# Kernel tuning notes

Hardware: AMD Instinct MI355X
Metric: run time of the kernel (lower is better)

Reference implementation:

```python
import jax, jax.numpy as jnp
import numpy as np

B, N, F_IN = 8, 4096, 32
NRP = 1024
D_MODEL = 512
K = 64  # max_num_neighbors
STAGE_CFG = ((1024, 0.05), (256, 0.3), (64, 0.5))  # (num_samples=ceil(0.25*N_in), radius)


def fps(pos, m):
    """Farthest point sampling of m points from pos (N,3), deterministic start at 0."""
    d = jnp.sum((pos - pos[0]) ** 2, axis=-1)
    idxs = jnp.zeros((m,), jnp.int32)
    def body(i, carry):
        idxs, d = carry
        nxt = jnp.argmax(d).astype(jnp.int32)
        d = jnp.minimum(d, jnp.sum((pos - pos[nxt]) ** 2, axis=-1))
        return (idxs.at[i].set(nxt), d)
    idxs, _ = jax.lax.fori_loop(1, m, body, (idxs, d))
    return idxs


def apply_mlp(h, ws, bs):
    for w, b in zip(ws[:-1], bs[:-1]):
        h = jax.nn.relu(h @ w + b)
    return h @ ws[-1] + bs[-1]


def sa_stage(x, pos, m, r, ws, bs):
    """SAModule: FPS -> radius neighbors (<=K) -> PointNetConv (gather, MLP, max-scatter)."""
    idx = jax.vmap(lambda p: fps(p, m))(pos)                          # (B,m)
    pos_s = jnp.take_along_axis(pos, idx[..., None], axis=1)          # (B,m,3)
    d2 = jnp.sum((pos_s[:, :, None, :] - pos[:, None, :, :]) ** 2, -1)  # (B,m,N)
    neg = jnp.where(d2 <= r * r, -d2, -jnp.inf)
    vals, nbr = jax.lax.top_k(neg, K)                                 # (B,m,K) nearest within r
    valid = vals > -jnp.inf                                           # self always valid (d2=0)
    x_j = jax.vmap(lambda xb, nb: xb[nb])(x, nbr)                     # (B,m,K,F) gather
    p_j = jax.vmap(lambda pb, nb: pb[nb])(pos, nbr)                   # (B,m,K,3)
    h = jnp.concatenate([x_j, p_j - pos_s[:, :, None, :]], axis=-1)   # message input
    h = apply_mlp(h, ws, bs)
    h = jnp.where(valid[..., None], h, -jnp.inf)
    return jnp.max(h, axis=2), pos_s                                  # max aggregation


def _forward(point_cloud_features, point_cloud, emb_table, point_id_emb, stage_params):
    x = emb_table[point_cloud_features[..., 0]]                       # (B,N,F_IN)
    x = x.at[:, :NRP].add(point_id_emb)
    pos = point_cloud
    for (m, r), (ws, bs) in zip(STAGE_CFG, stage_params):
        x, pos = sa_stage(x, pos, m, r, ws, bs)
    return x, pos                                                     # (B,64,D_MODEL), (B,64,3)


def setup_inputs() -> dict:
    key = jax.random.key(0)
    ks = iter(jax.random.split(key, 64))
    def nrm(shape, s=0.05):
        return s * jax.random.normal(next(ks), shape, dtype=jnp.float32)
    inp = {
        "point_cloud_features": jax.random.randint(next(ks), (B, N, 1), 0, 3),
        "point_cloud": jax.random.uniform(next(ks), (B, N, 3), dtype=jnp.float32),
        "emb_table": nrm((3, F_IN), 1.0),
        "point_id_emb": nrm((1, NRP, F_IN), 1.0),
    }
    dims = {"s1": [3 + F_IN, 64, 64, 64], "s2": [64 + 3, 128, 128, 256], "s3": [256 + 3, 256, 512, D_MODEL]}
    for s, d in dims.items():
        for i in range(3):
            inp[f"{s}w{i}"] = nrm((d[i], d[i + 1]))
            inp[f"{s}b{i}"] = jnp.zeros((d[i + 1],), jnp.float32)
    return inp


def reference(point_cloud_features, point_cloud, emb_table, point_id_emb,
              s1w0, s1b0, s1w1, s1b1, s1w2, s1b2,
              s2w0, s2b0, s2w1, s2b1, s2w2, s2b2,
              s3w0, s3b0, s3w1, s3b1, s3w2, s3b2):
    stage_params = [
        ([s1w0, s1w1, s1w2], [s1b0, s1b1, s1b2]),
        ([s2w0, s2w1, s2w2], [s2b0, s2b1, s2b2]),
        ([s3w0, s3w1, s3w2], [s3b0, s3b1, s3b2]),
    ]
    return _forward(point_cloud_features, point_cloud, emb_table, point_id_emb, stage_params)
```

## Files before the change

kernel.cpp:

```cpp
#include <hip/hip_runtime.h>

#define DEVI static __device__ __forceinline__

constexpr int B = 8;
constexpr int N0 = 4096;
constexpr int KNB = 64;

typedef float f32x2 __attribute__((ext_vector_type(2)));
typedef float f32x4 __attribute__((ext_vector_type(4)));
typedef short bf16x8 __attribute__((ext_vector_type(8)));

DEVI float dist2f(float ax, float ay, float az, float bx, float by, float bz) {
#pragma clang fp contract(off)
  float dx = ax - bx;
  float dy = ay - by;
  float dz = az - bz;
  return (dx * dx + dy * dy) + dz * dz;
}
DEVI f32x2 dist2v(f32x2 ax, f32x2 ay, f32x2 az, float bx, float by, float bz) {
#pragma clang fp contract(off)
  f32x2 dx = ax - bx;
  f32x2 dy = ay - by;
  f32x2 dz = az - bz;
  return (dx * dx + dy * dy) + dz * dz;
}

DEVI unsigned long long packMinKey(float v, int i) {
  return ((unsigned long long)__float_as_uint(v) << 32) | (unsigned int)i;
}

template <int CTRL, int RM>
DEVI float dppMaxF32(float v) {
  int o = __builtin_amdgcn_update_dpp(__float_as_int(v), __float_as_int(v),
                                      CTRL, RM, 0xf, false);
  return fmaxf(v, __int_as_float(o));
}
DEVI float waveMaxF32(float v) {
  v = dppMaxF32<0x111, 0xf>(v);
  v = dppMaxF32<0x112, 0xf>(v);
  v = dppMaxF32<0x114, 0xf>(v);
  v = dppMaxF32<0x118, 0xf>(v);
  v = dppMaxF32<0x142, 0xa>(v);
  v = dppMaxF32<0x143, 0xc>(v);
  return __int_as_float(__builtin_amdgcn_readlane(__float_as_int(v), 63));
}
template <int CTRL, int RM>
DEVI unsigned dppMinU32(unsigned v) {
  int o = __builtin_amdgcn_update_dpp((int)v, (int)v, CTRL, RM, 0xf, false);
  unsigned ov = (unsigned)o;
  return v < ov ? v : ov;
}
DEVI unsigned waveMinU32(unsigned v) {
  v = dppMinU32<0x111, 0xf>(v);
  v = dppMinU32<0x112, 0xf>(v);
  v = dppMinU32<0x114, 0xf>(v);
  v = dppMinU32<0x118, 0xf>(v);
  v = dppMinU32<0x142, 0xa>(v);
  v = dppMinU32<0x143, 0xc>(v);
  return (unsigned)__builtin_amdgcn_readlane((int)v, 63);
}

DEVI unsigned short bfhi(float x) {
  unsigned u = __float_as_uint(x);
  return (unsigned short)((u + 0x7FFFu + ((u >> 16) & 1u)) >> 16);
}
DEVI float bf2f(unsigned short h) { return __uint_as_float(((unsigned)h) << 16); }
DEVI void mkfrag(const float* p, bf16x8& hi, bf16x8& lo) {
#pragma unroll
  for (int e = 0; e < 8; ++e) {
    float x = p[e];
    unsigned short h = bfhi(x);
    float r = x - bf2f(h);
    unsigned short l2 = bfhi(r);
    hi[e] = (short)h;
    lo[e] = (short)l2;
  }
}


DEVI void x0_body(const int* __restrict__ feat, const float* __restrict__ emb,
                  const float* __restrict__ pid, float* __restrict__ x0buf,
                  int bx, int t) {
  int gid = bx * 256 + t;
  if (gid >= B * N0 * 32) return;
  int c = gid & 31;
  int bn = gid >> 5;
  int n = bn & (N0 - 1);
  int f = feat[bn];
  float v = emb[f * 32 + c];
  if (n < 1024) v += pid[n * 32 + c];
  x0buf[gid] = v;
}

template <int NPTS, int M, int BLK>
DEVI void fps_body(char* smem, const float* __restrict__ pos,
                   float* __restrict__ pos_out, int b, int t) {
  constexpr int EPT = NPTS / BLK;
  constexpr int EP2 = EPT / 2;
  constexpr int NW = BLK / 64;
  float4* posl = (float4*)smem;
  float4* outp = (float4*)(smem + (size_t)NPTS * 16);
  unsigned long long* redk =
      (unsigned long long*)(smem + (size_t)(NPTS + M) * 16);
  const float* pb = pos + (size_t)b * NPTS * 3;
  f32x2 px[EP2], py[EP2], pz[EP2], d[EP2];
#pragma unroll
  for (int e = 0; e < EP2; ++e) {
    int i0 = t + (2 * e) * BLK;
    int i1 = t + (2 * e + 1) * BLK;
    float x0 = pb[i0 * 3 + 0], y0 = pb[i0 * 3 + 1], z0 = pb[i0 * 3 + 2];
    float x1 = pb[i1 * 3 + 0], y1 = pb[i1 * 3 + 1], z1 = pb[i1 * 3 + 2];
    px[e] = (f32x2){x0, x1};
    py[e] = (f32x2){y0, y1};
    pz[e] = (f32x2){z0, z1};
    posl[i0] = make_float4(x0, y0, z0, 0.f);
    posl[i1] = make_float4(x1, y1, z1, 0.f);
  }
  float sx = pb[0], sy = pb[1], sz = pb[2];
  if (t == 0) outp[0] = make_float4(sx, sy, sz, 0.f);
  f32x2 m2 = (f32x2){-1.f, -1.f};
#pragma unroll
  for (int e = 0; e < EP2; ++e) {
    d[e] = dist2v(px[e], py[e], pz[e], sx, sy, sz);
    m2.x = fmaxf(m2.x, d[e].x);
    m2.y = fmaxf(m2.y, d[e].y);
  }
  for (int it = 1; it < M; ++it) {
    const float vstar = waveMaxF32(fmaxf(m2.x, m2.y));
    unsigned cand = 0xffffffffu;
#pragma unroll
    for (int e = 0; e < EP2; ++e) {
      unsigned c0 = (d[e].x == vstar) ? (unsigned)(t + (2 * e) * BLK) : 0xffffffffu;
      unsigned c1 = (d[e].y == vstar) ? (unsigned)(t + (2 * e + 1) * BLK) : 0xffffffffu;
      cand = cand < c0 ? cand : c0;
      cand = cand < c1 ? cand : c1;
    }
    cand = waveMinU32(cand);
    unsigned sel;
    if constexpr (NW > 1) {
      if ((t & 63) == 0) {
        unsigned long long key =
            ((unsigned long long)__float_as_uint(vstar) << 32) |
            (unsigned)(0x7fffffffu - cand);
        redk[(it & 1) * NW + (t >> 6)] = key;
      }
      __syncthreads();
      unsigned long long kk = redk[(it & 1) * NW + 0];
#pragma unroll
      for (int w = 1; w < NW; ++w) {
        unsigned long long o = redk[(it & 1) * NW + w];
        kk = (kk > o) ? kk : o;
      }
      sel = 0x7fffffffu - (unsigned)(kk & 0xffffffffULL);
    } else {
      sel = cand;
    }
    float4 sp = posl[sel];
    if (t == 0) outp[it] = sp;
    m2 = (f32x2){-1.f, -1.f};
#pragma unroll
    for (int e = 0; e < EP2; ++e) {
      f32x2 nd = dist2v(px[e], py[e], pz[e], sp.x, sp.y, sp.z);
      d[e].x = fminf(d[e].x, nd.x);
      d[e].y = fminf(d[e].y, nd.y);
      m2.x = fmaxf(m2.x, d[e].x);
      m2.y = fmaxf(m2.y, d[e].y);
    }
  }
  if constexpr (NW > 1) __syncthreads();
  for (int m = t; m < M; m += BLK) {
    float4 q = outp[m];
    pos_out[(size_t)(b * M + m) * 3 + 0] = q.x;
    pos_out[(size_t)(b * M + m) * 3 + 1] = q.y;
    pos_out[(size_t)(b * M + m) * 3 + 2] = q.z;
  }
}

template <int NPTS, int M>
DEVI void radius_body(char* smem, const float* __restrict__ pos,
                      const float* __restrict__ pos_s, float r2,
                      int* __restrict__ nbr, int* __restrict__ cnt, int blk,
                      int t) {
  unsigned long long* candkey = (unsigned long long*)smem;
  int* ctrp = (int*)(smem + (size_t)NPTS * 8);
  const int b = blk / M;
  const float* pb = pos + (size_t)b * NPTS * 3;
  const float cx = pos_s[(size_t)blk * 3 + 0];
  const float cy = pos_s[(size_t)blk * 3 + 1];
  const float cz = pos_s[(size_t)blk * 3 + 2];
  if (t == 0) *ctrp = 0;
  __syncthreads();
  for (int j = t; j < NPTS; j += 256) {
    float d2 = dist2f(pb[j * 3 + 0], pb[j * 3 + 1], pb[j * 3 + 2], cx, cy, cz);
    if (d2 <= r2) {
      int p = atomicAdd(ctrp, 1);
      candkey[p] = packMinKey(d2, j);
      if (p < KNB) nbr[(size_t)blk * KNB + p] = j;
    }
  }
  __syncthreads();
  const int c = *ctrp;
  if (c <= KNB) {
    if (t == 0) cnt[blk] = c;
    return;
  }
  for (int s = t; s < c; s += 256) {
    unsigned long long mykey = candkey[s];
    int rank = 0;
#pragma unroll 4
    for (int j = 0; j < c; ++j) {
      rank += (candkey[j] < mykey) ? 1 : 0;
    }
    if (rank < KNB)
      nbr[(size_t)blk * KNB + rank] = (int)(unsigned)(mykey & 0xffffffffULL);
  }
  if (t == 0) cnt[blk] = KNB;
}

DEVI void conv1_body(char* smem, const float* __restrict__ x0buf,
                     const float* __restrict__ pos,
                     const float* __restrict__ pos_s,
                     const int* __restrict__ nbr, const int* __restrict__ cntp,
                     const float* __restrict__ w0, const float* __restrict__ b0,
                     const float* __restrict__ w1, const float* __restrict__ b1,
                     const float* __restrict__ w2, const float* __restrict__ b2,
                     float* __restrict__ x1, int blk, int t) {
  float(*ins)[36] = (float(*)[36])smem;
  float(*hh)[65] = (float(*)[65])(smem + 576);
  float(*sred)[65] = (float(*)[65])(smem + 1616);
  const int slot = t >> 6;
  const int ch = t & 63;
  const int b = blk >> 10;
  const int c = cntp[blk];
  const float cx = pos_s[(size_t)blk * 3 + 0];
  const float cy = pos_s[(size_t)blk * 3 + 1];
  const float cz = pos_s[(size_t)blk * 3 + 2];
  float best = -__builtin_inff();
  for (int r0 = 0; r0 < c; r0 += 4) {
    const int r = r0 + slot;
    const bool act = r < c;
    const int j = nbr[(size_t)blk * KNB + (act ? r : 0)];
    if (ch < 32) {
      ins[slot][ch] = x0buf[((size_t)(b * N0) + j) * 32 + ch];
    } else if (ch < 35) {
      float pv = pos[((size_t)(b * N0) + j) * 3 + (ch - 32)];
      float cv = (ch == 32) ? cx : (ch == 33) ? cy : cz;
      ins[slot][ch] = pv - cv;
    }
    __syncthreads();
    float v = b0[ch];
#pragma unroll
    for (int i = 0; i < 35; ++i) v = fmaf(ins[slot][i], w0[i * 64 + ch], v);
    v = fmaxf(v, 0.f);
    hh[slot][ch] = v;
    __syncthreads();
    float v2 = b1[ch];
#pragma unroll
    for (int i = 0; i < 64; ++i) v2 = fmaf(hh[slot][i], w1[i * 64 + ch], v2);
    v2 = fmaxf(v2, 0.f);
    __syncthreads();
    hh[slot][ch] = v2;
    __syncthreads();
    float v3 = b2[ch];
#pragma unroll
    for (int i = 0; i < 64; ++i) v3 = fmaf(hh[slot][i], w2[i * 64 + ch], v3);
    if (act) best = fmaxf(best, v3);
    __syncthreads();
  }
  sred[slot][ch] = best;
  __syncthreads();
  if (t < 64) {
    float v = sred[0][t];
#pragma unroll
    for (int s = 1; s < 4; ++s) v = fmaxf(v, sred[s][t]);
    x1[(size_t)blk * 64 + t] = v;
  }
}

DEVI void conv2_mfma_body(char* smem, const float* __restrict__ x1,
                          const float* __restrict__ pos1,
                          const float* __restrict__ pos2,
                          const int* __restrict__ nbr,
                          const int* __restrict__ cntp,
                          const unsigned short* __restrict__ w0h,
                          const float* __restrict__ b0,
                          const unsigned short* __restrict__ w1h,
                          const float* __restrict__ b1,
                          const unsigned short* __restrict__ w2h,
                          const float* __restrict__ b2,
                          float* __restrict__ x2, int blk, int t) {
  float(*h1)[132] = (float(*)[132])smem;
  float(*h2)[132] = (float(*)[132])(smem + 33792);
  float* red = (float*)smem;
  const int b = blk >> 8;
  const int c = cntp[blk];
  const int w = t >> 6;
  const int lane = t & 63;
  const int cb = lane & 15;
  const int kb = lane >> 4;
  const int mrow = w * 16 + cb;
  const int jrow = nbr[(size_t)blk * KNB + (mrow < c ? mrow : c - 1)];
  const float* xrow = x1 + ((size_t)(b * 1024) + jrow) * 64;
  const float cx = pos2[(size_t)blk * 3 + 0];
  const float cy = pos2[(size_t)blk * 3 + 1];
  const float cz = pos2[(size_t)blk * 3 + 2];

  f32x4 acc1[8];
#pragma unroll
  for (int nt = 0; nt < 8; ++nt) acc1[nt] = (f32x4){0.f, 0.f, 0.f, 0.f};
#pragma unroll
  for (int ks = 0; ks < 2; ++ks) {
    float xv[8];
    *(float4*)&xv[0] = *(const float4*)&xrow[ks * 32 + kb * 8];
    *(float4*)&xv[4] = *(const float4*)&xrow[ks * 32 + kb * 8 + 4];
    bf16x8 ahi, alo;
    mkfrag(xv, ahi, alo);
#pragma unroll
    for (int nt = 0; nt < 8; ++nt) {
      size_t off = ((size_t)(nt * 3 + ks) * 64 + lane) * 8;
      bf16x8 bhi = *(const bf16x8*)(w0h + off);
      acc1[nt] = __builtin_amdgcn_mfma_f32_16x16x32_bf16(ahi, bhi, acc1[nt], 0, 0, 0);
      acc1[nt] = __builtin_amdgcn_mfma_f32_16x16x32_bf16(alo, bhi, acc1[nt], 0, 0, 0);
    }
  }
  {
    float xv[8] = {0.f, 0.f, 0.f, 0.f, 0.f, 0.f, 0.f, 0.f};
    if (kb == 0) {
      xv[0] = pos1[((size_t)(b * 1024) + jrow) * 3 + 0] - cx;
      xv[1] = pos1[((size_t)(b * 1024) + jrow) * 3 + 1] - cy;
      xv[2] = pos1[((size_t)(b * 1024) + jrow) * 3 + 2] - cz;
    }
    bf16x8 ahi, alo;
    mkfrag(xv, ahi, alo);
#pragma unroll
    for (int nt = 0; nt < 8; ++nt) {
      size_t off = ((size_t)(nt * 3 + 2) * 64 + lane) * 8;
      bf16x8 bhi = *(const bf16x8*)(w0h + off);
      acc1[nt] = __builtin_amdgcn_mfma_f32_16x16x32_bf16(ahi, bhi, acc1[nt], 0, 0, 0);
      acc1[nt] = __builtin_amdgcn_mfma_f32_16x16x32_bf16(alo, bhi, acc1[nt], 0, 0, 0);
    }
  }
  {
    const int mw = w * 16 + kb * 4;
#pragma unroll
    for (int nt = 0; nt < 8; ++nt) {
      float bias = b0[nt * 16 + cb];
#pragma unroll
      for (int r = 0; r < 4; ++r)
        h1[mw + r][nt * 16 + cb] = fmaxf(acc1[nt][r] + bias, 0.f);
    }
  }
  __syncthreads();

  f32x4 acc2[8];
#pragma unroll
  for (int nt = 0; nt < 8; ++nt) acc2[nt] = (f32x4){0.f, 0.f, 0.f, 0.f};
#pragma unroll
  for (int ks = 0; ks < 4; ++ks) {
    bf16x8 ahi, alo;
    mkfrag(&h1[mrow][ks * 32 + kb * 8], ahi, alo);
#pragma unroll
    for (int nt = 0; nt < 8; ++nt) {
      size_t off = ((size_t)(nt * 4 + ks) * 64 + lane) * 8;
      bf16x8 bhi = *(const bf16x8*)(w1h + off);
      acc2[nt] = __builtin_amdgcn_mfma_f32_16x16x32_bf16(ahi, bhi, acc2[nt], 0, 0, 0);
      acc2[nt] = __builtin_amdgcn_mfma_f32_16x16x32_bf16(alo, bhi, acc2[nt], 0, 0, 0);
    }
  }
  {
    const int mw = w * 16 + kb * 4;
#pragma unroll
    for (int nt = 0; nt < 8; ++nt) {
      float bias = b1[nt * 16 + cb];
#pragma unroll
      for (int r = 0; r < 4; ++r)
        h2[mw + r][nt * 16 + cb] = fmaxf(acc2[nt][r] + bias, 0.f);
    }
  }
  __syncthreads();

  f32x4 acc3[16];
#pragma unroll
  for (int nt = 0; nt < 16; ++nt) acc3[nt] = (f32x4){0.f, 0.f, 0.f, 0.f};
#pragma unroll
  for (int ks = 0; ks < 4; ++ks) {
    bf16x8 ahi, alo;
    mkfrag(&h2[mrow][ks * 32 + kb * 8], ahi, alo);
#pragma unroll
    for (int nt = 0; nt < 16; ++nt) {
      size_t off = ((size_t)(nt * 4 + ks) * 64 + lane) * 8;
      bf16x8 bhi = *(const bf16x8*)(w2h + off);
      acc3[nt] = __builtin_amdgcn_mfma_f32_16x16x32_bf16(ahi, bhi, acc3[nt], 0, 0, 0);
      acc3[nt] = __builtin_amdgcn_mfma_f32_16x16x32_bf16(alo, bhi, acc3[nt], 0, 0, 0);
    }
  }
  __syncthreads();
  {
    const int mw = w * 16 + kb * 4;
#pragma unroll
    for (int nt = 0; nt < 16; ++nt) {
      float bias = b2[nt * 16 + cb];
      float mx = -__builtin_inff();
#pragma unroll
      for (int r = 0; r < 4; ++r) {
        if (mw + r < c) mx = fmaxf(mx, acc3[nt][r] + bias);
      }
      red[(w * 4 + kb) * 256 + nt * 16 + cb] = mx;
    }
  }
  __syncthreads();
  {
    float v = red[t];
#pragma unroll
    for (int g = 1; g < 16; ++g) v = fmaxf(v, red[g * 256 + t]);
    x2[(size_t)blk * 256 + t] = v;
  }
}


__global__ void __launch_bounds__(256) l1_kernel(
    const float* __restrict__ pos, float* __restrict__ pos1,
    const int* __restrict__ feat, const float* __restrict__ emb,
    const float* __restrict__ pid, float* __restrict__ x0buf) {
  __shared__ __attribute__((aligned(16))) char smem[81984];
  if (blockIdx.x < 8) {
    fps_body<4096, 1024, 256>(smem, pos, pos1, blockIdx.x, threadIdx.x);
  } else {
    x0_body(feat, emb, pid, x0buf, blockIdx.x - 8, threadIdx.x);
  }
}

__global__ void __launch_bounds__(256) l2_kernel(
    const float* __restrict__ pos1, float* __restrict__ pos2,
    const float* __restrict__ pos, float r2a, int* __restrict__ nbr1,
    int* __restrict__ cnt1) {
  __shared__ __attribute__((aligned(16))) char smem[33024];
  if (blockIdx.x < 8) {
    fps_body<1024, 256, 256>(smem, pos1, pos2, blockIdx.x, threadIdx.x);
  } else {
    radius_body<4096, 1024>(smem, pos, pos1, r2a, nbr1, cnt1, blockIdx.x - 8,
                            threadIdx.x);
  }
}

__global__ void __launch_bounds__(256) l3_kernel(
    const float* __restrict__ pos2, float* __restrict__ pos3, float r2b,
    int* __restrict__ nbr2, int* __restrict__ cnt2,
    const float* __restrict__ pos1, const float* __restrict__ x0buf,
    const float* __restrict__ pos, const int* __restrict__ nbr1,
    const int* __restrict__ cnt1, const float* __restrict__ w0,
    const float* __restrict__ b0, const float* __restrict__ w1,
    const float* __restrict__ b1, const float* __restrict__ w2,
    const float* __restrict__ b2, float* __restrict__ x1) {
  __shared__ __attribute__((aligned(16))) char smem[8448];
  if (blockIdx.x < 8) {
    if (threadIdx.x < 64)
      fps_body<256, 64, 64>(smem, pos2, pos3, blockIdx.x, threadIdx.x);
  } else if (blockIdx.x < 8 + 2048) {
    radius_body<1024, 256>(smem, pos1, pos2, r2b, nbr2, cnt2, blockIdx.x - 8,
                           threadIdx.x);
  } else {
    conv1_body(smem, x0buf, pos, pos1, nbr1, cnt1, w0, b0, w1, b1, w2, b2, x1,
               blockIdx.x - (8 + 2048), threadIdx.x);
  }
}

__global__ void __launch_bounds__(256) l4_kernel(
    const float* __restrict__ pos2, const float* __restrict__ pos3, float r2c,
    int* __restrict__ nbr3, int* __restrict__ cnt3,
    const float* __restrict__ x1, const float* __restrict__ pos1,
    const int* __restrict__ nbr2, const int* __restrict__ cnt2,
    const unsigned short* __restrict__ v0h, const float* __restrict__ b0,
    const unsigned short* __restrict__ v1h, const float* __restrict__ b1,
    const unsigned short* __restrict__ v2h, const float* __restrict__ b2,
    float* __restrict__ x2) {
  __shared__ __attribute__((aligned(16))) char smem[67584];
  if (blockIdx.x < 512) {
    radius_body<256, 64>(smem, pos2, pos3, r2c, nbr3, cnt3, blockIdx.x,
                         threadIdx.x);
  } else {
    conv2_mfma_body(smem, x1, pos1, pos2, nbr2, cnt2, v0h, b0, v1h, b1, v2h,
                    b2, x2, blockIdx.x - 512, threadIdx.x);
  }
}

__global__ void __launch_bounds__(256) pack_kernel(
    const float* __restrict__ W, int Kreal, int KS, int N,
    unsigned short* __restrict__ hi, unsigned short* __restrict__ lo) {
  int gid = blockIdx.x * 256 + threadIdx.x;
  int total = (N / 16) * KS * 64 * 8;
  if (gid >= total) return;
  int e = gid & 7;
  int l = (gid >> 3) & 63;
  int rest = gid >> 9;
  int ks = rest % KS;
  int nt = rest / KS;
  int n = nt * 16 + (l & 15);
  int k = ks * 32 + (l >> 4) * 8 + e;
  float val = (k < Kreal) ? W[(size_t)k * N + n] : 0.f;
  unsigned short h = bfhi(val);
  float r = val - bf2f(h);
  hi[gid] = h;
  lo[gid] = bfhi(r);
}

__global__ void __launch_bounds__(256) conv3_mfma(
    const float* __restrict__ x2, const float* __restrict__ pos2,
    const float* __restrict__ pos3, const int* __restrict__ nbr,
    const int* __restrict__ cntp,
    const unsigned short* __restrict__ w0h, const unsigned short* __restrict__ w0l,
    const float* __restrict__ b0,
    const unsigned short* __restrict__ w1h, const unsigned short* __restrict__ w1l,
    const float* __restrict__ b1,
    const unsigned short* __restrict__ w2h, const unsigned short* __restrict__ w2l,
    const float* __restrict__ b2, float* __restrict__ out) {
  __shared__ __attribute__((aligned(16))) float h1s[64 * 268];
  __shared__ __attribute__((aligned(16))) float h2cs[64 * 140];
  __shared__ __attribute__((aligned(16))) float msgcs[64 * 44];
  const int blk = blockIdx.x;
  const int t = threadIdx.x;
  const int b = blk >> 6;
  const int c = cntp[blk];
  const int w = t >> 6;
  const int lane = t & 63;
  const int cb = lane & 15;
  const int kb = lane >> 4;
  const float cx = pos3[(size_t)blk * 3 + 0];
  const float cy = pos3[(size_t)blk * 3 + 1];
  const float cz = pos3[(size_t)blk * 3 + 2];
  const int mrow = w * 16 + cb;

  f32x4 acc1[16];
#pragma unroll
  for (int nt = 0; nt < 16; ++nt) acc1[nt] = (f32x4){0.f, 0.f, 0.f, 0.f};
  for (int ks = 0; ks < 9; ++ks) {
#pragma unroll
    for (int i = 0; i < 8; ++i) {
      int idx = t + i * 256;
      int row = idx >> 5;
      int col = idx & 31;
      int kg = ks * 32 + col;
      int j = nbr[(size_t)blk * KNB + (row < c ? row : c - 1)];
      float v = 0.f;
      if (kg < 256) {
        v = x2[((size_t)(b * 256) + j) * 256 + kg];
      } else if (kg < 259) {
        float pv = pos2[((size_t)(b * 256) + j) * 3 + (kg - 256)];
        v = pv - ((kg == 256) ? cx : (kg == 257) ? cy : cz);
      }
      msgcs[row * 44 + col] = v;
    }
    __syncthreads();
    bf16x8 ahi, alo;
    mkfrag(&msgcs[mrow * 44 + kb * 8], ahi, alo);
#pragma unroll
    for (int nt = 0; nt < 16; ++nt) {
      size_t off = ((size_t)(nt * 9 + ks) * 64 + lane) * 8;
      bf16x8 bhi = *(const bf16x8*)(w0h + off);
      bf16x8 blo = *(const bf16x8*)(w0l + off);
      acc1[nt] = __builtin_amdgcn_mfma_f32_16x16x32_bf16(ahi, bhi, acc1[nt], 0, 0, 0);
      acc1[nt] = __builtin_amdgcn_mfma_f32_16x16x32_bf16(alo, bhi, acc1[nt], 0, 0, 0);
      acc1[nt] = __builtin_amdgcn_mfma_f32_16x16x32_bf16(ahi, blo, acc1[nt], 0, 0, 0);
    }
    __syncthreads();
  }
  {
    const int mw = w * 16 + kb * 4;
#pragma unroll
    for (int nt = 0; nt < 16; ++nt) {
      float bias = b0[nt * 16 + cb];
#pragma unroll
      for (int r = 0; r < 4; ++r)
        h1s[(mw + r) * 268 + nt * 16 + cb] = fmaxf(acc1[nt][r] + bias, 0.f);
    }
  }
  __syncthreads();

  f32x4 acc3[32];
#pragma unroll
  for (int nt = 0; nt < 32; ++nt) acc3[nt] = (f32x4){0.f, 0.f, 0.f, 0.f};
  for (int ch = 0; ch < 4; ++ch) {
    f32x4 acc2[8];
#pragma unroll
    for (int nt = 0; nt < 8; ++nt) acc2[nt] = (f32x4){0.f, 0.f, 0.f, 0.f};
#pragma unroll
    for (int ks = 0; ks < 8; ++ks) {
      bf16x8 ahi, alo;
      mkfrag(&h1s[mrow * 268 + ks * 32 + kb * 8], ahi, alo);
#pragma unroll
      for (int nt = 0; nt < 8; ++nt) {
        size_t off = ((size_t)((ch * 8 + nt) * 8 + ks) * 64 + lane) * 8;
        bf16x8 bhi = *(const bf16x8*)(w1h + off);
        bf16x8 blo = *(const bf16x8*)(w1l + off);
        acc2[nt] = __builtin_amdgcn_mfma_f32_16x16x32_bf16(ahi, bhi, acc2[nt], 0, 0, 0);
        acc2[nt] = __builtin_amdgcn_mfma_f32_16x16x32_bf16(alo, bhi, acc2[nt], 0, 0, 0);
        acc2[nt] = __builtin_amdgcn_mfma_f32_16x16x32_bf16(ahi, blo, acc2[nt], 0, 0, 0);
      }
    }
    {
      const int mw = w * 16 + kb * 4;
#pragma unroll
      for (int nt = 0; nt < 8; ++nt) {
        float bias = b1[ch * 128 + nt * 16 + cb];
#pragma unroll
        for (int r = 0; r < 4; ++r)
          h2cs[(mw + r) * 140 + nt * 16 + cb] = fmaxf(acc2[nt][r] + bias, 0.f);
      }
    }
    __syncthreads();
#pragma unroll
    for (int ks3 = 0; ks3 < 4; ++ks3) {
      bf16x8 ahi, alo;
      mkfrag(&h2cs[mrow * 140 + ks3 * 32 + kb * 8], ahi, alo);
#pragma unroll
      for (int nt = 0; nt < 32; ++nt) {
        size_t off = ((size_t)(nt * 16 + ch * 4 + ks3) * 64 + lane) * 8;
        bf16x8 bhi = *(const bf16x8*)(w2h + off);
        bf16x8 blo = *(const bf16x8*)(w2l + off);
        acc3[nt] = __builtin_amdgcn_mfma_f32_16x16x32_bf16(ahi, bhi, acc3[nt], 0, 0, 0);
        acc3[nt] = __builtin_amdgcn_mfma_f32_16x16x32_bf16(alo, bhi, acc3[nt], 0, 0, 0);
        acc3[nt] = __builtin_amdgcn_mfma_f32_16x16x32_bf16(ahi, blo, acc3[nt], 0, 0, 0);
      }
    }
    __syncthreads();
  }

  float* redw = h1s;
  {
    const int mw = w * 16 + kb * 4;
#pragma unroll
    for (int nt = 0; nt < 32; ++nt) {
      float bias = b2[nt * 16 + cb];
      float mx = -__builtin_inff();
#pragma unroll
      for (int r = 0; r < 4; ++r) {
        if (mw + r < c) mx = fmaxf(mx, acc3[nt][r] + bias);
      }
      redw[(w * 4 + kb) * 512 + nt * 16 + cb] = mx;
    }
  }
  __syncthreads();
#pragma unroll
  for (int half = 0; half < 2; ++half) {
    int col = t + half * 256;
    float v = redw[col];
#pragma unroll
    for (int g = 1; g < 16; ++g) v = fmaxf(v, redw[g * 512 + col]);
    out[(size_t)blk * 512 + col] = v;
  }
}

extern "C" void kernel_launch(void* const* d_in, const int* in_sizes, int n_in,
                              void* d_out, int out_size, void* d_ws, size_t ws_size,
                              hipStream_t stream) {
  const int* feat = (const int*)d_in[0];
  const float* pos = (const float*)d_in[1];
  const float* emb = (const float*)d_in[2];
  const float* pid = (const float*)d_in[3];
  const float* s1w0 = (const float*)d_in[4];
  const float* s1b0 = (const float*)d_in[5];
  const float* s1w1 = (const float*)d_in[6];
  const float* s1b1 = (const float*)d_in[7];
  const float* s1w2 = (const float*)d_in[8];
  const float* s1b2 = (const float*)d_in[9];
  const float* s2w0 = (const float*)d_in[10];
  const float* s2b0 = (const float*)d_in[11];
  const float* s2w1 = (const float*)d_in[12];
  const float* s2b1 = (const float*)d_in[13];
  const float* s2w2 = (const float*)d_in[14];
  const float* s2b2 = (const float*)d_in[15];
  const float* s3w0 = (const float*)d_in[16];
  const float* s3b0 = (const float*)d_in[17];
  const float* s3w1 = (const float*)d_in[18];
  const float* s3b1 = (const float*)d_in[19];
  const float* s3w2 = (const float*)d_in[20];
  const float* s3b2 = (const float*)d_in[21];
  (void)in_sizes; (void)n_in; (void)out_size; (void)ws_size;

  char* ws = (char*)d_ws;
  size_t off = 0;
  auto alloc = [&](size_t nbytes) {
    void* p = ws + off;
    off = (off + nbytes + 255) & ~(size_t)255;
    return p;
  };
  float* x0 = (float*)alloc((size_t)B * N0 * 32 * 4);
  float* pos1 = (float*)alloc((size_t)B * 1024 * 3 * 4);
  int* nbr1 = (int*)alloc((size_t)B * 1024 * KNB * 4);
  int* cnt1 = (int*)alloc((size_t)B * 1024 * 4);
  float* x1 = (float*)alloc((size_t)B * 1024 * 64 * 4);
  float* pos2 = (float*)alloc((size_t)B * 256 * 3 * 4);
  int* nbr2 = (int*)alloc((size_t)B * 256 * KNB * 4);
  int* cnt2 = (int*)alloc((size_t)B * 256 * 4);
  float* x2 = (float*)alloc((size_t)B * 256 * 256 * 4);
  int* nbr3 = (int*)alloc((size_t)B * 64 * KNB * 4);
  int* cnt3 = (int*)alloc((size_t)B * 64 * 4);
  const int T0 = 16 * 9 * 64 * 8;
  const int T1 = 32 * 8 * 64 * 8;
  const int T2 = 32 * 16 * 64 * 8;
  unsigned short* w0h = (unsigned short*)alloc((size_t)T0 * 2);
  unsigned short* w0l = (unsigned short*)alloc((size_t)T0 * 2);
  unsigned short* w1h = (unsigned short*)alloc((size_t)T1 * 2);
  unsigned short* w1l = (unsigned short*)alloc((size_t)T1 * 2);
  unsigned short* w2h = (unsigned short*)alloc((size_t)T2 * 2);
  unsigned short* w2l = (unsigned short*)alloc((size_t)T2 * 2);
  const int U0 = 8 * 3 * 64 * 8;
  const int U1 = 8 * 4 * 64 * 8;
  const int U2 = 16 * 4 * 64 * 8;
  unsigned short* v0h = (unsigned short*)alloc((size_t)U0 * 2);
  unsigned short* v0l = (unsigned short*)alloc((size_t)U0 * 2);
  unsigned short* v1h = (unsigned short*)alloc((size_t)U1 * 2);
  unsigned short* v1l = (unsigned short*)alloc((size_t)U1 * 2);
  unsigned short* v2h = (unsigned short*)alloc((size_t)U2 * 2);
  unsigned short* v2l = (unsigned short*)alloc((size_t)U2 * 2);

  float* xout = (float*)d_out;
  float* pos3 = xout + (size_t)B * 64 * 512;

  const float r2a = (float)(0.05 * 0.05);
  const float r2b = (float)(0.3 * 0.3);
  const float r2c = (float)(0.5 * 0.5);

  pack_kernel<<<(T0 + 255) / 256, 256, 0, stream>>>(s3w0, 259, 9, 256, w0h, w0l);
  pack_kernel<<<(T1 + 255) / 256, 256, 0, stream>>>(s3w1, 256, 8, 512, w1h, w1l);
  pack_kernel<<<(T2 + 255) / 256, 256, 0, stream>>>(s3w2, 512, 16, 512, w2h, w2l);
  pack_kernel<<<(U0 + 255) / 256, 256, 0, stream>>>(s2w0, 67, 3, 128, v0h, v0l);
  pack_kernel<<<(U1 + 255) / 256, 256, 0, stream>>>(s2w1, 128, 4, 128, v1h, v1l);
  pack_kernel<<<(U2 + 255) / 256, 256, 0, stream>>>(s2w2, 128, 4, 256, v2h, v2l);

  l1_kernel<<<8 + 4096, 256, 0, stream>>>(pos, pos1, feat, emb, pid, x0);
  l2_kernel<<<8 + 8192, 256, 0, stream>>>(pos1, pos2, pos, r2a, nbr1, cnt1);
  l3_kernel<<<8 + 2048 + 8192, 256, 0, stream>>>(
      pos2, pos3, r2b, nbr2, cnt2, pos1, x0, pos, nbr1, cnt1,
      s1w0, s1b0, s1w1, s1b1, s1w2, s1b2, x1);
  l4_kernel<<<512 + 2048, 256, 0, stream>>>(
      pos2, pos3, r2c, nbr3, cnt3, x1, pos1, nbr2, cnt2,
      v0h, s2b0, v1h, s2b1, v2h, s2b2, x2);
  conv3_mfma<<<B * 64, 256, 0, stream>>>(x2, pos2, pos3, nbr3, cnt3,
                                         w0h, w0l, s3b0, w1h, w1l, s3b1,
                                         w2h, w2l, s3b2, xout);
}
```

Before: 1.327 ms.

## Drop weight low-part MFMAs in conv3, load activations directly, remove block barriers

Stage-3 conv drops the bf16 low-part weight term, going from three MFMAs per tile to two (hi/lo split of activations only). The shared-memory message staging buffer goes away: each lane now reads its own neighbor row straight from global memory into the A fragment. Several __syncthreads are also removed in conv3 and in the stage-2 kernel, on the basis that each wave reads only rows it wrote itself. Together these cut MFMA count, weight traffic and barrier stalls, at the cost of lower weight precision and reliance on wave-private LDS rows.

```diff
diff --git a/kernel.cpp b/kernel.cpp
--- a/kernel.cpp
+++ b/kernel.cpp
@@ -350,7 +350,6 @@
         h1[mw + r][nt * 16 + cb] = fmaxf(acc1[nt][r] + bias, 0.f);
     }
   }
-  __syncthreads();
 
   f32x4 acc2[8];
 #pragma unroll
@@ -377,7 +376,6 @@
         h2[mw + r][nt * 16 + cb] = fmaxf(acc2[nt][r] + bias, 0.f);
     }
   }
-  __syncthreads();
 
   f32x4 acc3[16];
 #pragma unroll
@@ -508,15 +506,12 @@
     const float* __restrict__ x2, const float* __restrict__ pos2,
     const float* __restrict__ pos3, const int* __restrict__ nbr,
     const int* __restrict__ cntp,
-    const unsigned short* __restrict__ w0h, const unsigned short* __restrict__ w0l,
-    const float* __restrict__ b0,
-    const unsigned short* __restrict__ w1h, const unsigned short* __restrict__ w1l,
-    const float* __restrict__ b1,
-    const unsigned short* __restrict__ w2h, const unsigned short* __restrict__ w2l,
-    const float* __restrict__ b2, float* __restrict__ out) {
+    const unsigned short* __restrict__ w0h, const float* __restrict__ b0,
+    const unsigned short* __restrict__ w1h, const float* __restrict__ b1,
+    const unsigned short* __restrict__ w2h, const float* __restrict__ b2,
+    float* __restrict__ out) {
   __shared__ __attribute__((aligned(16))) float h1s[64 * 268];
   __shared__ __attribute__((aligned(16))) float h2cs[64 * 140];
-  __shared__ __attribute__((aligned(16))) float msgcs[64 * 44];
   const int blk = blockIdx.x;
   const int t = threadIdx.x;
   const int b = blk >> 6;
@@ -529,40 +524,43 @@
   const float cy = pos3[(size_t)blk * 3 + 1];
   const float cz = pos3[(size_t)blk * 3 + 2];
   const int mrow = w * 16 + cb;
+  const int jrow = nbr[(size_t)blk * KNB + (mrow < c ? mrow : c - 1)];
+  const float* xrow = x2 + ((size_t)(b * 256) + jrow) * 256;
 
   f32x4 acc1[16];
 #pragma unroll
   for (int nt = 0; nt < 16; ++nt) acc1[nt] = (f32x4){0.f, 0.f, 0.f, 0.f};
-  for (int ks = 0; ks < 9; ++ks) {
-#pragma unroll
-    for (int i = 0; i < 8; ++i) {
-      int idx = t + i * 256;
-      int row = idx >> 5;
-      int col = idx & 31;
-      int kg = ks * 32 + col;
-      int j = nbr[(size_t)blk * KNB + (row < c ? row : c - 1)];
-      float v = 0.f;
-      if (kg < 256) {
-        v = x2[((size_t)(b * 256) + j) * 256 + kg];
-      } else if (kg < 259) {
-        float pv = pos2[((size_t)(b * 256) + j) * 3 + (kg - 256)];
-        v = pv - ((kg == 256) ? cx : (kg == 257) ? cy : cz);
-      }
-      msgcs[row * 44 + col] = v;
-    }
-    __syncthreads();
+#pragma unroll
+  for (int ks = 0; ks < 8; ++ks) {
+    float xv[8];
+    *(float4*)&xv[0] = *(const float4*)&xrow[ks * 32 + kb * 8];
+    *(float4*)&xv[4] = *(const float4*)&xrow[ks * 32 + kb * 8 + 4];
     bf16x8 ahi, alo;
-    mkfrag(&msgcs[mrow * 44 + kb * 8], ahi, alo);
+    mkfrag(xv, ahi, alo);
 #pragma unroll
     for (int nt = 0; nt < 16; ++nt) {
       size_t off = ((size_t)(nt * 9 + ks) * 64 + lane) * 8;
       bf16x8 bhi = *(const bf16x8*)(w0h + off);
-      bf16x8 blo = *(const bf16x8*)(w0l + off);
       acc1[nt] = __builtin_amdgcn_mfma_f32_16x16x32_bf16(ahi, bhi, acc1[nt], 0, 0, 0);
       acc1[nt] = __builtin_amdgcn_mfma_f32_16x16x32_bf16(alo, bhi, acc1[nt], 0, 0, 0);
-      acc1[nt] = __builtin_amdgcn_mfma_f32_16x16x32_bf16(ahi, blo, acc1[nt], 0, 0, 0);
-    }
-    __syncthreads();
+    }
+  }
+  {
+    float xv[8] = {0.f, 0.f, 0.f, 0.f, 0.f, 0.f, 0.f, 0.f};
+    if (kb == 0) {
+      xv[0] = pos2[((size_t)(b * 256) + jrow) * 3 + 0] - cx;
+      xv[1] = pos2[((size_t)(b * 256) + jrow) * 3 + 1] - cy;
+      xv[2] = pos2[((size_t)(b * 256) + jrow) * 3 + 2] - cz;
+    }
+    bf16x8 ahi, alo;
+    mkfrag(xv, ahi, alo);
+#pragma unroll
+    for (int nt = 0; nt < 16; ++nt) {
+      size_t off = ((size_t)(nt * 9 + 8) * 64 + lane) * 8;
+      bf16x8 bhi = *(const bf16x8*)(w0h + off);
+      acc1[nt] = __builtin_amdgcn_mfma_f32_16x16x32_bf16(ahi, bhi, acc1[nt], 0, 0, 0);
+      acc1[nt] = __builtin_amdgcn_mfma_f32_16x16x32_bf16(alo, bhi, acc1[nt], 0, 0, 0);
+    }
   }
   {
     const int mw = w * 16 + kb * 4;
@@ -574,7 +572,6 @@
         h1s[(mw + r) * 268 + nt * 16 + cb] = fmaxf(acc1[nt][r] + bias, 0.f);
     }
   }
-  __syncthreads();
 
   f32x4 acc3[32];
 #pragma unroll
@@ -591,10 +588,8 @@
       for (int nt = 0; nt < 8; ++nt) {
         size_t off = ((size_t)((ch * 8 + nt) * 8 + ks) * 64 + lane) * 8;
         bf16x8 bhi = *(const bf16x8*)(w1h + off);
-        bf16x8 blo = *(const bf16x8*)(w1l + off);
         acc2[nt] = __builtin_amdgcn_mfma_f32_16x16x32_bf16(ahi, bhi, acc2[nt], 0, 0, 0);
         acc2[nt] = __builtin_amdgcn_mfma_f32_16x16x32_bf16(alo, bhi, acc2[nt], 0, 0, 0);
-        acc2[nt] = __builtin_amdgcn_mfma_f32_16x16x32_bf16(ahi, blo, acc2[nt], 0, 0, 0);
       }
     }
     {
@@ -607,7 +602,6 @@
           h2cs[(mw + r) * 140 + nt * 16 + cb] = fmaxf(acc2[nt][r] + bias, 0.f);
       }
     }
-    __syncthreads();
 #pragma unroll
     for (int ks3 = 0; ks3 < 4; ++ks3) {
       bf16x8 ahi, alo;
@@ -616,15 +610,13 @@
       for (int nt = 0; nt < 32; ++nt) {
         size_t off = ((size_t)(nt * 16 + ch * 4 + ks3) * 64 + lane) * 8;
         bf16x8 bhi = *(const bf16x8*)(w2h + off);
-        bf16x8 blo = *(const bf16x8*)(w2l + off);
         acc3[nt] = __builtin_amdgcn_mfma_f32_16x16x32_bf16(ahi, bhi, acc3[nt], 0, 0, 0);
         acc3[nt] = __builtin_amdgcn_mfma_f32_16x16x32_bf16(alo, bhi, acc3[nt], 0, 0, 0);
-        acc3[nt] = __builtin_amdgcn_mfma_f32_16x16x32_bf16(ahi, blo, acc3[nt], 0, 0, 0);
       }
     }
-    __syncthreads();
-  }
-
+  }
+
+  __syncthreads();
   float* redw = h1s;
   {
     const int mw = w * 16 + kb * 4;
@@ -737,6 +729,5 @@
       pos2, pos3, r2c, nbr3, cnt3, x1, pos1, nbr2, cnt2,
       v0h, s2b0, v1h, s2b1, v2h, s2b2, x2);
   conv3_mfma<<<B * 64, 256, 0, stream>>>(x2, pos2, pos3, nbr3, cnt3,
-                                         w0h, w0l, s3b0, w1h, w1l, s3b1,
-                                         w2h, w2l, s3b2, xout);
-}
+                                         w0h, s3b0, w1h, s3b1, w2h, s3b2, xout);
+}
```

After: 1.280 ms. -3.6%, faster.
